# Optimization experiments

Measured on AMD Instinct MI355X. Metric: run time of the kernel, lower is better.

Reference implementation:

```python
import jax, jax.numpy as jnp
import numpy as np

N_NODES = 100000


def gcn_conv(x, edge_index, W, b):
    """PyG GCNConv: symmetric normalization with added self-loops.
    x: [N, Fin], edge_index: [2, E], W: [Fin, Fout], b: [Fout]
    """
    n = x.shape[0]
    h = x @ W  # [N, Fout] dense transform first (standard GCNConv order)
    loops = jnp.arange(n, dtype=edge_index.dtype)
    src = jnp.concatenate([edge_index[0], loops])  # self-loops appended
    dst = jnp.concatenate([edge_index[1], loops])
    deg = jax.ops.segment_sum(jnp.ones_like(dst, dtype=h.dtype), dst, num_segments=n)
    dinv = jax.lax.rsqrt(deg)  # deg >= 1 thanks to self-loops
    norm = dinv[src] * dinv[dst]  # [E+N]
    msgs = h[src] * norm[:, None]  # gather + scale
    out = jax.ops.segment_sum(msgs, dst, num_segments=n)  # scatter-add
    return out + b


def setup_inputs() -> dict:
    key = jax.random.key(0)
    k = jax.random.split(key, 9)
    in_c, hid, out_c = 128, 128, 64
    n_edges = 1600000
    x = jax.random.normal(k[0], (N_NODES, in_c), dtype=jnp.float32)
    edge_index = jax.random.randint(k[1], (2, n_edges), 0, N_NODES, dtype=jnp.int64)
    def lin(kw, kb, fan_in, fan_out):
        bound = 1.0 / np.sqrt(fan_in)
        W = jax.random.uniform(kw, (fan_in, fan_out), jnp.float32, -bound, bound)
        b = jax.random.uniform(kb, (fan_out,), jnp.float32, -bound, bound)
        return W, b
    W1, b1 = lin(k[2], k[3], in_c, hid)
    W2, b2 = lin(k[4], k[5], hid, hid)
    Wf, bf = lin(k[6], k[7], hid, out_c)
    return {"x": x, "edge_index": edge_index, "W1": W1, "b1": b1,
            "W2": W2, "b2": b2, "Wf": Wf, "bf": bf}


def reference(x, edge_index, W1, b1, W2, b2, Wf, bf):
    h = jax.nn.relu(gcn_conv(x, edge_index, W1, b1))
    h = jax.nn.relu(gcn_conv(h, edge_index, W2, b2))
    return h @ Wf + bf
```

## Files before the change

### kernel.cpp

```cpp
#include <hip/hip_runtime.h>
#include <stdint.h>

typedef short short8 __attribute__((ext_vector_type(8)));
typedef float floatx4 __attribute__((ext_vector_type(4)));

#define BK 256

static __device__ __forceinline__ float bflo(unsigned int u) {
    union { unsigned int i; float f; } v; v.i = u << 16; return v.f;
}
static __device__ __forceinline__ float bfhi(unsigned int u) {
    union { unsigned int i; float f; } v; v.i = u & 0xffff0000u; return v.f;
}
static __device__ __forceinline__ unsigned short f2bf(float f) {
    union { float f; unsigned int i; } v; v.f = f;
    unsigned int u = v.i;
    unsigned int r = u + 0x7fffu + ((u >> 16) & 1u);
    return (unsigned short)(r >> 16);
}


__global__ void k_zero_cnt(int* bucket_cnt, int K) {
    int i = blockIdx.x * 256 + threadIdx.x;
    if (i < K) bucket_cnt[i] = 0;
}

__global__ __launch_bounds__(256) void k_hist(const int* __restrict__ dst, int* bucket_cnt,
                                              int E, int N, int K) {
    __shared__ int h[4][512];
    int t = threadIdx.x, w = t >> 6;
    for (int i = t; i < 4 * 512; i += 256) ((int*)h)[i] = 0;
    __syncthreads();
    int per = (E + gridDim.x - 1) / gridDim.x;
    int lo = blockIdx.x * per, hi = min(lo + per, E);
    for (int e = lo + t; e < hi; e += 256) {
        unsigned int d = (unsigned int)dst[e];
        if (d < (unsigned int)N) atomicAdd(&h[w][d >> 8], 1);
    }
    __syncthreads();
    for (int i = t; i < K; i += 256) {
        int c = h[0][i] + h[1][i] + h[2][i] + h[3][i];
        if (c) atomicAdd(&bucket_cnt[i], c);
    }
}

__global__ void k_scanK(const int* __restrict__ bucket_cnt, int* bucket_off, int* bucket_cur,
                        int* row_start, int K, int N) {
    __shared__ int s[512];
    int t = threadIdx.x;
    int v = (t < K) ? bucket_cnt[t] : 0;
    s[t] = v; __syncthreads();
    for (int off = 1; off < 512; off <<= 1) {
        int x = (t >= off) ? s[t - off] : 0;
        __syncthreads();
        s[t] += x;
        __syncthreads();
    }
    if (t < K) { bucket_off[t] = s[t] - v; bucket_cur[t] = s[t] - v; }
    if (t == K - 1) { bucket_off[K] = s[t]; row_start[N] = s[t]; }
}

__global__ __launch_bounds__(256) void k_binscatter(const int* __restrict__ src,
                                                    const int* __restrict__ dst,
                                                    int* bucket_cur, unsigned int* __restrict__ tmp,
                                                    int E, int N, int K) {
    __shared__ int h[4][512];
    int t = threadIdx.x, w = t >> 6;
    for (int i = t; i < 4 * 512; i += 256) ((int*)h)[i] = 0;
    __syncthreads();
    int per = (E + gridDim.x - 1) / gridDim.x;
    int lo = blockIdx.x * per, hi = min(lo + per, E);
    for (int e = lo + t; e < hi; e += 256) {
        unsigned int d = (unsigned int)dst[e];
        if (d < (unsigned int)N) atomicAdd(&h[w][d >> 8], 1);
    }
    __syncthreads();
    for (int k = t; k < K; k += 256) {
        int c0 = h[0][k], c1 = h[1][k], c2 = h[2][k], c3 = h[3][k];
        int tot = c0 + c1 + c2 + c3;
        int base = tot ? atomicAdd(&bucket_cur[k], tot) : 0;
        h[0][k] = base; h[1][k] = base + c0; h[2][k] = base + c0 + c1;
        h[3][k] = base + c0 + c1 + c2;
    }
    __syncthreads();
    for (int e = lo + t; e < hi; e += 256) {
        unsigned int d = (unsigned int)dst[e];
        if (d < (unsigned int)N) {
            unsigned int sv = (unsigned int)src[e];
            if (sv >= (unsigned int)N) sv = 0;
            int p = atomicAdd(&h[w][d >> 8], 1);
            tmp[p] = (sv << 8) | (d & 255u);
        }
    }
}

__global__ __launch_bounds__(256) void k_fine(const unsigned int* __restrict__ tmp,
                                              const int* __restrict__ bucket_off,
                                              int* __restrict__ row_start, float* __restrict__ dinv,
                                              int* __restrict__ csr, int N) {
    __shared__ int deg4[4][BK];
    __shared__ int scn[BK];
    __shared__ int cur[BK];
    int b = blockIdx.x, t = threadIdx.x, w = t >> 6;
    int lo = bucket_off[b], hi = bucket_off[b + 1];
    for (int i = t; i < 4 * BK; i += 256) ((int*)deg4)[i] = 0;
    __syncthreads();
    for (int e = lo + t; e < hi; e += 256) atomicAdd(&deg4[w][tmp[e] & 255u], 1);
    __syncthreads();
    int v = deg4[0][t] + deg4[1][t] + deg4[2][t] + deg4[3][t];
    scn[t] = v; __syncthreads();
    for (int off = 1; off < 256; off <<= 1) {
        int x = (t >= off) ? scn[t - off] : 0;
        __syncthreads();
        scn[t] += x;
        __syncthreads();
    }
    int rs = lo + scn[t] - v;
    cur[t] = rs;
    int node = b * BK + t;
    if (node < N) { row_start[node] = rs; dinv[node] = rsqrtf((float)(v + 1)); }
    __syncthreads();
    for (int e = lo + t; e < hi; e += 256) {
        unsigned int p = tmp[e];
        int pos = atomicAdd(&cur[p & 255u], 1);
        csr[pos] = (int)(p >> 8);
    }
}


__global__ void k_wconv_all(const float* __restrict__ W1, const float* __restrict__ W2,
                            const float* __restrict__ Wf, unsigned short* __restrict__ wb1,
                            unsigned short* __restrict__ wb2, unsigned short* __restrict__ wbf) {
    int i = blockIdx.x * 256 + threadIdx.x;
    if (i < 16384) {
        int k = i >> 7, n = i & 127;
        wb1[n * 128 + k] = f2bf(W1[i]);
    } else if (i < 32768) {
        int j = i - 16384, k = j >> 7, n = j & 127;
        wb2[n * 128 + k] = f2bf(W2[j]);
    } else if (i < 40960) {
        int j = i - 32768, k = j >> 6, n = j & 63;
        wbf[n * 128 + k] = f2bf(Wf[j]);
    }
}


template <int NOUT, bool SCALE, bool BIAS, bool XF32, bool OUTF32>
__global__ __launch_bounds__(256, 2) void k_gemm(
    const void* __restrict__ Xv, const unsigned short* __restrict__ Wbf,
    const float* __restrict__ bias, const float* __restrict__ dinv,
    void* __restrict__ outv, int M, int MB) {
    __shared__ __align__(16) unsigned short Wl[NOUT * 136];
    int t = threadIdx.x;
    for (int c = t; c < NOUT * 16; c += 256) {
        short8 v = *(const short8*)(Wbf + (size_t)c * 8);
        *(short8*)(&Wl[(c >> 4) * 136 + (c & 15) * 8]) = v;
    }
    __syncthreads();

    int wave = t >> 6, lane = t & 63;
    int quad = lane >> 4, l16 = lane & 15;
    constexpr int NT = NOUT / 16;

    for (int mb = blockIdx.x; mb < MB; mb += gridDim.x) {
        int m0 = mb * 64 + wave * 16;
        int mr = m0 + l16;
        int mrc = mr < M ? mr : M - 1;

        floatx4 acc[NT];
#pragma unroll
        for (int i = 0; i < NT; i++) acc[i] = (floatx4){0.f, 0.f, 0.f, 0.f};

#pragma unroll
        for (int kc = 0; kc < 4; kc++) {
            short8 a;
            if (XF32) {
                const float* X = (const float*)Xv;
                const float* p = X + (size_t)mrc * 128 + kc * 32 + quad * 8;
                float4 xa = *(const float4*)p;
                float4 xb = *(const float4*)(p + 4);
                a[0] = (short)f2bf(xa.x); a[1] = (short)f2bf(xa.y);
                a[2] = (short)f2bf(xa.z); a[3] = (short)f2bf(xa.w);
                a[4] = (short)f2bf(xb.x); a[5] = (short)f2bf(xb.y);
                a[6] = (short)f2bf(xb.z); a[7] = (short)f2bf(xb.w);
            } else {
                const unsigned short* X = (const unsigned short*)Xv;
                a = *(const short8*)(X + (size_t)mrc * 128 + kc * 32 + quad * 8);
            }
#pragma unroll
            for (int nt = 0; nt < NT; nt++) {
                short8 b = *(const short8*)(&Wl[(nt * 16 + l16) * 136 + kc * 32 + quad * 8]);
                acc[nt] = __builtin_amdgcn_mfma_f32_16x16x32_bf16(a, b, acc[nt], 0, 0, 0);
            }
        }

#pragma unroll
        for (int i = 0; i < 4; i++) {
            int r = m0 + quad * 4 + i;
            if (r >= M) continue;
            float sc = SCALE ? dinv[r] : 1.0f;
#pragma unroll
            for (int nt = 0; nt < NT; nt++) {
                int n = nt * 16 + l16;
                float v = acc[nt][i] * sc;
                if (BIAS) v += bias[n];
                if (OUTF32) {
                    ((float*)outv)[(size_t)r * NOUT + n] = v;
                } else {
                    ((unsigned short*)outv)[(size_t)r * NOUT + n] = f2bf(v);
                }
            }
        }
    }
}


__global__ __launch_bounds__(256, 8) void k_aggregate(
    const unsigned short* __restrict__ Hs, const int* __restrict__ csr,
    const int* __restrict__ row_start,
    const float* __restrict__ dinv, const float* __restrict__ bias,
    unsigned short* __restrict__ out, int N, int E) {
    int wave = threadIdx.x >> 6, lane = threadIdx.x & 63;
    int grp = lane >> 4, c16 = lane & 15;
    int node = blockIdx.x * 4 + wave;
    if (node >= N) return;
    int Nm1 = N - 1;
    int cb = c16 * 8;

    float a0 = 0.f, a1 = 0.f, a2 = 0.f, a3 = 0.f, a4 = 0.f, a5 = 0.f, a6 = 0.f, a7 = 0.f;

    int start = row_start[node];
    int end = row_start[node + 1];
    if (start < 0) start = 0;
    if (end > E) end = E;
    int cnt = end - start;
    int full4 = cnt >> 2;

    int it = 0;
    for (; it + 2 <= full4; it += 2) {
        int eA = start + it * 4 + grp;
        int eB = eA + 4;
        int iA = min(max(csr[eA], 0), Nm1);
        int iB = min(max(csr[eB], 0), Nm1);
        uint4 uA = *(const uint4*)(Hs + (size_t)iA * 128 + cb);
        uint4 uB = *(const uint4*)(Hs + (size_t)iB * 128 + cb);
        a0 += bflo(uA.x); a1 += bfhi(uA.x); a2 += bflo(uA.y); a3 += bfhi(uA.y);
        a4 += bflo(uA.z); a5 += bfhi(uA.z); a6 += bflo(uA.w); a7 += bfhi(uA.w);
        a0 += bflo(uB.x); a1 += bfhi(uB.x); a2 += bflo(uB.y); a3 += bfhi(uB.y);
        a4 += bflo(uB.z); a5 += bfhi(uB.z); a6 += bflo(uB.w); a7 += bfhi(uB.w);
    }
    for (; it < full4; it++) {
        int eA = start + it * 4 + grp;
        int iA = min(max(csr[eA], 0), Nm1);
        uint4 uA = *(const uint4*)(Hs + (size_t)iA * 128 + cb);
        a0 += bflo(uA.x); a1 += bfhi(uA.x); a2 += bflo(uA.y); a3 += bfhi(uA.y);
        a4 += bflo(uA.z); a5 += bfhi(uA.z); a6 += bflo(uA.w); a7 += bfhi(uA.w);
    }
    int eT = start + full4 * 4 + grp;
    if (eT < end) {
        int iT = min(max(csr[eT], 0), Nm1);
        uint4 uT = *(const uint4*)(Hs + (size_t)iT * 128 + cb);
        a0 += bflo(uT.x); a1 += bfhi(uT.x); a2 += bflo(uT.y); a3 += bfhi(uT.y);
        a4 += bflo(uT.z); a5 += bfhi(uT.z); a6 += bflo(uT.w); a7 += bfhi(uT.w);
    }

    a0 += __shfl_xor(a0, 16); a1 += __shfl_xor(a1, 16); a2 += __shfl_xor(a2, 16);
    a3 += __shfl_xor(a3, 16); a4 += __shfl_xor(a4, 16); a5 += __shfl_xor(a5, 16);
    a6 += __shfl_xor(a6, 16); a7 += __shfl_xor(a7, 16);
    a0 += __shfl_xor(a0, 32); a1 += __shfl_xor(a1, 32); a2 += __shfl_xor(a2, 32);
    a3 += __shfl_xor(a3, 32); a4 += __shfl_xor(a4, 32); a5 += __shfl_xor(a5, 32);
    a6 += __shfl_xor(a6, 32); a7 += __shfl_xor(a7, 32);

    uint4 us = *(const uint4*)(Hs + (size_t)node * 128 + cb);
    a0 += bflo(us.x); a1 += bfhi(us.x); a2 += bflo(us.y); a3 += bfhi(us.y);
    a4 += bflo(us.z); a5 += bfhi(us.z); a6 += bflo(us.w); a7 += bfhi(us.w);

    float di = dinv[node];
    float4 b0 = *(const float4*)(bias + cb);
    float4 b1 = *(const float4*)(bias + cb + 4);
    float r0 = fmaxf(fmaf(di, a0, b0.x), 0.f);
    float r1 = fmaxf(fmaf(di, a1, b0.y), 0.f);
    float r2 = fmaxf(fmaf(di, a2, b0.z), 0.f);
    float r3 = fmaxf(fmaf(di, a3, b0.w), 0.f);
    float r4 = fmaxf(fmaf(di, a4, b1.x), 0.f);
    float r5 = fmaxf(fmaf(di, a5, b1.y), 0.f);
    float r6 = fmaxf(fmaf(di, a6, b1.z), 0.f);
    float r7 = fmaxf(fmaf(di, a7, b1.w), 0.f);
    if (grp == 0) {
        uint4 o;
        o.x = (unsigned int)f2bf(r0) | ((unsigned int)f2bf(r1) << 16);
        o.y = (unsigned int)f2bf(r2) | ((unsigned int)f2bf(r3) << 16);
        o.z = (unsigned int)f2bf(r4) | ((unsigned int)f2bf(r5) << 16);
        o.w = (unsigned int)f2bf(r6) | ((unsigned int)f2bf(r7) << 16);
        *(uint4*)(out + (size_t)node * 128 + cb) = o;
    }
}


extern "C" void kernel_launch(void* const* d_in, const int* in_sizes, int n_in,
                              void* d_out, int out_size, void* d_ws, size_t ws_size,
                              hipStream_t stream) {
    const float* x  = (const float*)d_in[0];
    const int* ei   = (const int*)d_in[1];
    const float* W1 = (const float*)d_in[2];
    const float* b1 = (const float*)d_in[3];
    const float* W2 = (const float*)d_in[4];
    const float* b2 = (const float*)d_in[5];
    const float* Wf = (const float*)d_in[6];
    const float* bf = (const float*)d_in[7];

    int N = in_sizes[0] / 128;
    int E = in_sizes[1] / 2;
    const int* src = ei;
    const int* dst = ei + E;
    int K = (N + BK - 1) / BK;
    if (N >= (1 << 24) || K > 512) return;

    size_t need = 0;
    auto pad = [](size_t b) { return (b + 255) & ~(size_t)255; };
    size_t o_bcnt = need; need += pad(512 * 4);
    size_t o_boff = need; need += pad(513 * 4);
    size_t o_bcur = need; need += pad(512 * 4);
    size_t o_rs   = need; need += pad(((size_t)N + 1) * 4);
    size_t o_dinv = need; need += pad((size_t)N * 4);
    size_t o_wbf  = need; need += pad((16384 + 16384 + 8192) * 2);
    size_t o_csr  = need; need += pad((size_t)E * 4);
    size_t o_hs   = need; need += pad((size_t)N * 128 * 2);
    size_t o_a    = need; need += pad((size_t)N * 128 * 2);
    if (ws_size < need) return;
    if ((size_t)E * 4 > (size_t)N * 128 * 2) return;

    char* ws = (char*)d_ws;
    int* bucket_cnt = (int*)(ws + o_bcnt);
    int* bucket_off = (int*)(ws + o_boff);
    int* bucket_cur = (int*)(ws + o_bcur);
    int* row_start  = (int*)(ws + o_rs);
    float* dinv     = (float*)(ws + o_dinv);
    unsigned short* wb1 = (unsigned short*)(ws + o_wbf);
    unsigned short* wb2 = wb1 + 16384;
    unsigned short* wbf = wb2 + 16384;
    int* csr        = (int*)(ws + o_csr);
    unsigned short* Hs = (unsigned short*)(ws + o_hs);
    unsigned short* A  = (unsigned short*)(ws + o_a);
    unsigned int* tmp  = (unsigned int*)A;

    k_wconv_all<<<160, 256, 0, stream>>>(W1, W2, Wf, wb1, wb2, wbf);

    k_zero_cnt<<<2, 256, 0, stream>>>(bucket_cnt, 512);
    k_hist<<<256, 256, 0, stream>>>(dst, bucket_cnt, E, N, K);
    k_scanK<<<1, 512, 0, stream>>>(bucket_cnt, bucket_off, bucket_cur, row_start, K, N);
    k_binscatter<<<256, 256, 0, stream>>>(src, dst, bucket_cur, tmp, E, N, K);
    k_fine<<<K, 256, 0, stream>>>(tmp, bucket_off, row_start, dinv, csr, N);

    int MB = (N + 63) / 64;
    int GG = (MB + 1) / 2;

    k_gemm<128, true, false, true, false><<<GG, 256, 0, stream>>>(x, wb1, nullptr, dinv, Hs, N, MB);
    k_aggregate<<<(N + 3) / 4, 256, 0, stream>>>(Hs, csr, row_start, dinv, b1, A, N, E);
    k_gemm<128, true, false, false, false><<<GG, 256, 0, stream>>>(A, wb2, nullptr, dinv, Hs, N, MB);
    k_aggregate<<<(N + 3) / 4, 256, 0, stream>>>(Hs, csr, row_start, dinv, b2, A, N, E);
    k_gemm<64, false, true, false, true><<<GG, 256, 0, stream>>>(A, wbf, bf, nullptr, d_out, N, MB);
}
```

Before: 336.5 us.

## Preload CSR indices per wave and broadcast via shuffles in aggregate kernel

The aggregate kernel now loads up to 64 neighbor indices once per wave, one per lane, and hands them to the gathering lanes with __shfl. This removes the dependent per-iteration CSR loads that preceded each feature-row gather. The main loop is unrolled to four gathers in flight, the self-row load is hoisted ahead of the loop, accumulation uses packed float2 vectors, and addresses are built with 32-bit shift/or arithmetic. Rows with more than 64 neighbors fall back to a direct CSR loop, and the 32-bit offsets assume the feature buffer stays under 4 GB.

```diff
diff --git a/kernel.cpp b/kernel.cpp
--- a/kernel.cpp
+++ b/kernel.cpp
@@ -3,6 +3,7 @@
 
 typedef short short8 __attribute__((ext_vector_type(8)));
 typedef float floatx4 __attribute__((ext_vector_type(4)));
+typedef float f32x2 __attribute__((ext_vector_type(2)));
 
 #define BK 256
 
@@ -17,6 +18,11 @@
     unsigned int u = v.i;
     unsigned int r = u + 0x7fffu + ((u >> 16) & 1u);
     return (unsigned short)(r >> 16);
+}
+static __device__ __forceinline__ f32x2 unp2(unsigned int u) {
+    union { unsigned int i; float f; } lo, hi;
+    lo.i = u << 16; hi.i = u & 0xffff0000u;
+    f32x2 r; r.x = lo.f; r.y = hi.f; return r;
 }
 
 
@@ -225,44 +231,59 @@
     int node = blockIdx.x * 4 + wave;
     if (node >= N) return;
     int Nm1 = N - 1;
-    int cb = c16 * 8;
-
-    float a0 = 0.f, a1 = 0.f, a2 = 0.f, a3 = 0.f, a4 = 0.f, a5 = 0.f, a6 = 0.f, a7 = 0.f;
+    unsigned int cb2 = (unsigned int)c16 << 4;
+    const char* Hb = (const char*)Hs;
 
     int start = row_start[node];
     int end = row_start[node + 1];
     if (start < 0) start = 0;
     if (end > E) end = E;
     int cnt = end - start;
-    int full4 = cnt >> 2;
-
+
+    uint4 us = *(const uint4*)(Hb + (((size_t)node << 8) | cb2));
+
+    int pre = cnt < 64 ? cnt : 64;
+    int idxv = 0;
+    if (lane < pre) idxv = min(max(csr[start + lane], 0), Nm1);
+
+    f32x2 a01 = {0.f, 0.f}, a23 = {0.f, 0.f}, a45 = {0.f, 0.f}, a67 = {0.f, 0.f};
+#define ACC8(u) do { a01 += unp2((u).x); a23 += unp2((u).y); \
+                     a45 += unp2((u).z); a67 += unp2((u).w); } while (0)
+
+    int full4 = pre >> 2;
     int it = 0;
-    for (; it + 2 <= full4; it += 2) {
-        int eA = start + it * 4 + grp;
-        int eB = eA + 4;
-        int iA = min(max(csr[eA], 0), Nm1);
-        int iB = min(max(csr[eB], 0), Nm1);
-        uint4 uA = *(const uint4*)(Hs + (size_t)iA * 128 + cb);
-        uint4 uB = *(const uint4*)(Hs + (size_t)iB * 128 + cb);
-        a0 += bflo(uA.x); a1 += bfhi(uA.x); a2 += bflo(uA.y); a3 += bfhi(uA.y);
-        a4 += bflo(uA.z); a5 += bfhi(uA.z); a6 += bflo(uA.w); a7 += bfhi(uA.w);
-        a0 += bflo(uB.x); a1 += bfhi(uB.x); a2 += bflo(uB.y); a3 += bfhi(uB.y);
-        a4 += bflo(uB.z); a5 += bfhi(uB.z); a6 += bflo(uB.w); a7 += bfhi(uB.w);
+    for (; it + 4 <= full4; it += 4) {
+        int p = it * 4 + grp;
+        int i0 = __shfl(idxv, p);
+        int i1 = __shfl(idxv, p + 4);
+        int i2 = __shfl(idxv, p + 8);
+        int i3 = __shfl(idxv, p + 12);
+        uint4 u0 = *(const uint4*)(Hb + (((unsigned int)i0 << 8) | cb2));
+        uint4 u1 = *(const uint4*)(Hb + (((unsigned int)i1 << 8) | cb2));
+        uint4 u2 = *(const uint4*)(Hb + (((unsigned int)i2 << 8) | cb2));
+        uint4 u3 = *(const uint4*)(Hb + (((unsigned int)i3 << 8) | cb2));
+        ACC8(u0); ACC8(u1); ACC8(u2); ACC8(u3);
     }
     for (; it < full4; it++) {
-        int eA = start + it * 4 + grp;
-        int iA = min(max(csr[eA], 0), Nm1);
-        uint4 uA = *(const uint4*)(Hs + (size_t)iA * 128 + cb);
-        a0 += bflo(uA.x); a1 += bfhi(uA.x); a2 += bflo(uA.y); a3 += bfhi(uA.y);
-        a4 += bflo(uA.z); a5 += bfhi(uA.z); a6 += bflo(uA.w); a7 += bfhi(uA.w);
-    }
-    int eT = start + full4 * 4 + grp;
-    if (eT < end) {
-        int iT = min(max(csr[eT], 0), Nm1);
-        uint4 uT = *(const uint4*)(Hs + (size_t)iT * 128 + cb);
-        a0 += bflo(uT.x); a1 += bfhi(uT.x); a2 += bflo(uT.y); a3 += bfhi(uT.y);
-        a4 += bflo(uT.z); a5 += bfhi(uT.z); a6 += bflo(uT.w); a7 += bfhi(uT.w);
-    }
+        int i0 = __shfl(idxv, it * 4 + grp);
+        uint4 u0 = *(const uint4*)(Hb + (((unsigned int)i0 << 8) | cb2));
+        ACC8(u0);
+    }
+    int eT = full4 * 4 + grp;
+    int iT = __shfl(idxv, eT < pre ? eT : 0);
+    if (eT < pre) {
+        uint4 u0 = *(const uint4*)(Hb + (((unsigned int)iT << 8) | cb2));
+        ACC8(u0);
+    }
+    for (int e = start + 64 + grp; e < end; e += 4) {
+        int ii = min(max(csr[e], 0), Nm1);
+        uint4 u = *(const uint4*)(Hb + (((unsigned int)ii << 8) | cb2));
+        ACC8(u);
+    }
+#undef ACC8
+
+    float a0 = a01.x, a1 = a01.y, a2 = a23.x, a3 = a23.y;
+    float a4 = a45.x, a5 = a45.y, a6 = a67.x, a7 = a67.y;
 
     a0 += __shfl_xor(a0, 16); a1 += __shfl_xor(a1, 16); a2 += __shfl_xor(a2, 16);
     a3 += __shfl_xor(a3, 16); a4 += __shfl_xor(a4, 16); a5 += __shfl_xor(a5, 16);
@@ -271,13 +292,12 @@
     a3 += __shfl_xor(a3, 32); a4 += __shfl_xor(a4, 32); a5 += __shfl_xor(a5, 32);
     a6 += __shfl_xor(a6, 32); a7 += __shfl_xor(a7, 32);
 
-    uint4 us = *(const uint4*)(Hs + (size_t)node * 128 + cb);
     a0 += bflo(us.x); a1 += bfhi(us.x); a2 += bflo(us.y); a3 += bfhi(us.y);
     a4 += bflo(us.z); a5 += bfhi(us.z); a6 += bflo(us.w); a7 += bfhi(us.w);
 
     float di = dinv[node];
-    float4 b0 = *(const float4*)(bias + cb);
-    float4 b1 = *(const float4*)(bias + cb + 4);
+    float4 b0 = *(const float4*)(bias + c16 * 8);
+    float4 b1 = *(const float4*)(bias + c16 * 8 + 4);
     float r0 = fmaxf(fmaf(di, a0, b0.x), 0.f);
     float r1 = fmaxf(fmaf(di, a1, b0.y), 0.f);
     float r2 = fmaxf(fmaf(di, a2, b0.z), 0.f);
@@ -292,7 +312,7 @@
         o.y = (unsigned int)f2bf(r2) | ((unsigned int)f2bf(r3) << 16);
         o.z = (unsigned int)f2bf(r4) | ((unsigned int)f2bf(r5) << 16);
         o.w = (unsigned int)f2bf(r6) | ((unsigned int)f2bf(r7) << 16);
-        *(uint4*)(out + (size_t)node * 128 + cb) = o;
+        *(uint4*)(out + (((size_t)node << 7) | (size_t)(c16 * 8))) = o;
     }
 }
 
```

Result: no change. 335.9 us (-0.2%).

## Store features in 16-column slices and aggregate per slice for cache locality

Applied to the files above, without the earlier changes.

Changes the intermediate feature layout to eight column slices of 16 bf16 values per node. The GEMMs write and read this sliced layout, and the new aggregation kernel launches one block per (node chunk, slice) so each gather touches a 3.2MB slice that fits in cache better. Each lane takes a different edge and the results are combined with a 16-lane shuffle reduction. The change also folds the bucket-count zeroing into the weight-conversion kernel to save a launch. In exchange, the CSR indices are re-read once per slice (8x index traffic), the GEMM stores become strided, and there is more shuffle work.

```diff
diff --git a/kernel.cpp b/kernel.cpp
--- a/kernel.cpp
+++ b/kernel.cpp
@@ -20,9 +20,22 @@
 }
 
 
-__global__ void k_zero_cnt(int* bucket_cnt, int K) {
+__global__ void k_wconv_all(const float* __restrict__ W1, const float* __restrict__ W2,
+                            const float* __restrict__ Wf, unsigned short* __restrict__ wb1,
+                            unsigned short* __restrict__ wb2, unsigned short* __restrict__ wbf,
+                            int* __restrict__ bucket_cnt) {
     int i = blockIdx.x * 256 + threadIdx.x;
-    if (i < K) bucket_cnt[i] = 0;
+    if (i < 512) bucket_cnt[i] = 0;
+    if (i < 16384) {
+        int k = i >> 7, n = i & 127;
+        wb1[n * 128 + k] = f2bf(W1[i]);
+    } else if (i < 32768) {
+        int j = i - 16384, k = j >> 7, n = j & 127;
+        wb2[n * 128 + k] = f2bf(W2[j]);
+    } else if (i < 40960) {
+        int j = i - 32768, k = j >> 6, n = j & 63;
+        wbf[n * 128 + k] = f2bf(Wf[j]);
+    }
 }
 
 __global__ __launch_bounds__(256) void k_hist(const int* __restrict__ dst, int* bucket_cnt,
@@ -128,24 +141,7 @@
 }
 
 
-__global__ void k_wconv_all(const float* __restrict__ W1, const float* __restrict__ W2,
-                            const float* __restrict__ Wf, unsigned short* __restrict__ wb1,
-                            unsigned short* __restrict__ wb2, unsigned short* __restrict__ wbf) {
-    int i = blockIdx.x * 256 + threadIdx.x;
-    if (i < 16384) {
-        int k = i >> 7, n = i & 127;
-        wb1[n * 128 + k] = f2bf(W1[i]);
-    } else if (i < 32768) {
-        int j = i - 16384, k = j >> 7, n = j & 127;
-        wb2[n * 128 + k] = f2bf(W2[j]);
-    } else if (i < 40960) {
-        int j = i - 32768, k = j >> 6, n = j & 63;
-        wbf[n * 128 + k] = f2bf(Wf[j]);
-    }
-}
-
-
-template <int NOUT, bool SCALE, bool BIAS, bool XF32, bool OUTF32>
+template <int NOUT, bool SCALE, bool BIAS, bool XF32, bool XSLICED, bool OUTF32, bool OSLICED>
 __global__ __launch_bounds__(256, 2) void k_gemm(
     const void* __restrict__ Xv, const unsigned short* __restrict__ Wbf,
     const float* __restrict__ bias, const float* __restrict__ dinv,
@@ -183,6 +179,10 @@
                 a[2] = (short)f2bf(xa.z); a[3] = (short)f2bf(xa.w);
                 a[4] = (short)f2bf(xb.x); a[5] = (short)f2bf(xb.y);
                 a[6] = (short)f2bf(xb.z); a[7] = (short)f2bf(xb.w);
+            } else if (XSLICED) {
+                const unsigned short* X = (const unsigned short*)Xv;
+                int sl = kc * 2 + (quad >> 1);
+                a = *(const short8*)(X + ((size_t)sl * M + mrc) * 16 + (quad & 1) * 8);
             } else {
                 const unsigned short* X = (const unsigned short*)Xv;
                 a = *(const short8*)(X + (size_t)mrc * 128 + kc * 32 + quad * 8);
@@ -206,6 +206,8 @@
                 if (BIAS) v += bias[n];
                 if (OUTF32) {
                     ((float*)outv)[(size_t)r * NOUT + n] = v;
+                } else if (OSLICED) {
+                    ((unsigned short*)outv)[((size_t)nt * M + r) * 16 + l16] = f2bf(v);
                 } else {
                     ((unsigned short*)outv)[(size_t)r * NOUT + n] = f2bf(v);
                 }
@@ -215,84 +217,93 @@
 }
 
 
-__global__ __launch_bounds__(256, 8) void k_aggregate(
+__global__ __launch_bounds__(256, 8) void k_agg_slice(
     const unsigned short* __restrict__ Hs, const int* __restrict__ csr,
-    const int* __restrict__ row_start,
-    const float* __restrict__ dinv, const float* __restrict__ bias,
-    unsigned short* __restrict__ out, int N, int E) {
-    int wave = threadIdx.x >> 6, lane = threadIdx.x & 63;
-    int grp = lane >> 4, c16 = lane & 15;
-    int node = blockIdx.x * 4 + wave;
-    if (node >= N) return;
+    const int* __restrict__ row_start, const float* __restrict__ dinv,
+    const float* __restrict__ bias, unsigned short* __restrict__ out, int N, int E) {
+    int s = blockIdx.x & 7, chunk = blockIdx.x >> 3;
+    int t = threadIdx.x;
+    int wave = t >> 6, lane = t & 63, sub = lane >> 4, el = lane & 15;
     int Nm1 = N - 1;
-    int cb = c16 * 8;
-
-    float a0 = 0.f, a1 = 0.f, a2 = 0.f, a3 = 0.f, a4 = 0.f, a5 = 0.f, a6 = 0.f, a7 = 0.f;
-
-    int start = row_start[node];
-    int end = row_start[node + 1];
-    if (start < 0) start = 0;
-    if (end > E) end = E;
-    int cnt = end - start;
-    int full4 = cnt >> 2;
-
-    int it = 0;
-    for (; it + 2 <= full4; it += 2) {
-        int eA = start + it * 4 + grp;
-        int eB = eA + 4;
-        int iA = min(max(csr[eA], 0), Nm1);
-        int iB = min(max(csr[eB], 0), Nm1);
-        uint4 uA = *(const uint4*)(Hs + (size_t)iA * 128 + cb);
-        uint4 uB = *(const uint4*)(Hs + (size_t)iB * 128 + cb);
-        a0 += bflo(uA.x); a1 += bfhi(uA.x); a2 += bflo(uA.y); a3 += bfhi(uA.y);
-        a4 += bflo(uA.z); a5 += bfhi(uA.z); a6 += bflo(uA.w); a7 += bfhi(uA.w);
-        a0 += bflo(uB.x); a1 += bfhi(uB.x); a2 += bflo(uB.y); a3 += bfhi(uB.y);
-        a4 += bflo(uB.z); a5 += bfhi(uB.z); a6 += bflo(uB.w); a7 += bfhi(uB.w);
-    }
-    for (; it < full4; it++) {
-        int eA = start + it * 4 + grp;
-        int iA = min(max(csr[eA], 0), Nm1);
-        uint4 uA = *(const uint4*)(Hs + (size_t)iA * 128 + cb);
-        a0 += bflo(uA.x); a1 += bfhi(uA.x); a2 += bflo(uA.y); a3 += bfhi(uA.y);
-        a4 += bflo(uA.z); a5 += bfhi(uA.z); a6 += bflo(uA.w); a7 += bfhi(uA.w);
-    }
-    int eT = start + full4 * 4 + grp;
-    if (eT < end) {
-        int iT = min(max(csr[eT], 0), Nm1);
-        uint4 uT = *(const uint4*)(Hs + (size_t)iT * 128 + cb);
-        a0 += bflo(uT.x); a1 += bfhi(uT.x); a2 += bflo(uT.y); a3 += bfhi(uT.y);
-        a4 += bflo(uT.z); a5 += bfhi(uT.z); a6 += bflo(uT.w); a7 += bfhi(uT.w);
-    }
-
-    a0 += __shfl_xor(a0, 16); a1 += __shfl_xor(a1, 16); a2 += __shfl_xor(a2, 16);
-    a3 += __shfl_xor(a3, 16); a4 += __shfl_xor(a4, 16); a5 += __shfl_xor(a5, 16);
-    a6 += __shfl_xor(a6, 16); a7 += __shfl_xor(a7, 16);
-    a0 += __shfl_xor(a0, 32); a1 += __shfl_xor(a1, 32); a2 += __shfl_xor(a2, 32);
-    a3 += __shfl_xor(a3, 32); a4 += __shfl_xor(a4, 32); a5 += __shfl_xor(a5, 32);
-    a6 += __shfl_xor(a6, 32); a7 += __shfl_xor(a7, 32);
-
-    uint4 us = *(const uint4*)(Hs + (size_t)node * 128 + cb);
-    a0 += bflo(us.x); a1 += bfhi(us.x); a2 += bflo(us.y); a3 += bfhi(us.y);
-    a4 += bflo(us.z); a5 += bfhi(us.z); a6 += bflo(us.w); a7 += bfhi(us.w);
-
-    float di = dinv[node];
-    float4 b0 = *(const float4*)(bias + cb);
-    float4 b1 = *(const float4*)(bias + cb + 4);
-    float r0 = fmaxf(fmaf(di, a0, b0.x), 0.f);
-    float r1 = fmaxf(fmaf(di, a1, b0.y), 0.f);
-    float r2 = fmaxf(fmaf(di, a2, b0.z), 0.f);
-    float r3 = fmaxf(fmaf(di, a3, b0.w), 0.f);
-    float r4 = fmaxf(fmaf(di, a4, b1.x), 0.f);
-    float r5 = fmaxf(fmaf(di, a5, b1.y), 0.f);
-    float r6 = fmaxf(fmaf(di, a6, b1.z), 0.f);
-    float r7 = fmaxf(fmaf(di, a7, b1.w), 0.f);
-    if (grp == 0) {
-        uint4 o;
-        o.x = (unsigned int)f2bf(r0) | ((unsigned int)f2bf(r1) << 16);
-        o.y = (unsigned int)f2bf(r2) | ((unsigned int)f2bf(r3) << 16);
-        o.z = (unsigned int)f2bf(r4) | ((unsigned int)f2bf(r5) << 16);
-        o.w = (unsigned int)f2bf(r6) | ((unsigned int)f2bf(r7) << 16);
-        *(uint4*)(out + (size_t)node * 128 + cb) = o;
+    const unsigned short* Hsl = Hs + (size_t)s * N * 16;
+    unsigned short* Osl = out + (size_t)s * N * 16;
+
+    const float* bsl = bias + s * 16;
+    float4 q0 = *(const float4*)(bsl);
+    float4 q1 = *(const float4*)(bsl + 4);
+    float4 q2 = *(const float4*)(bsl + 8);
+    float4 q3 = *(const float4*)(bsl + 12);
+
+    int nb = chunk * 64 + wave * 16 + sub;
+#pragma unroll 1
+    for (int p = 0; p < 4; ++p) {
+        int node = nb + p * 4;
+        int node_c = node < N ? node : Nm1;
+        int start = row_start[node_c];
+        int end = row_start[node_c + 1];
+        if (start < 0) start = 0;
+        if (end > E) end = E;
+
+        float a0 = 0.f, a1 = 0.f, a2 = 0.f, a3 = 0.f, a4 = 0.f, a5 = 0.f, a6 = 0.f, a7 = 0.f;
+        float a8 = 0.f, a9 = 0.f, a10 = 0.f, a11 = 0.f, a12 = 0.f, a13 = 0.f, a14 = 0.f, a15 = 0.f;
+
+        for (int e = start + el; e < end; e += 16) {
+            unsigned int ii = (unsigned int)csr[e];
+            if (ii >= (unsigned int)N) ii = 0;
+            const uint4* rp = (const uint4*)(Hsl + (size_t)ii * 16);
+            uint4 ua = rp[0], ub = rp[1];
+            a0 += bflo(ua.x); a1 += bfhi(ua.x); a2 += bflo(ua.y); a3 += bfhi(ua.y);
+            a4 += bflo(ua.z); a5 += bfhi(ua.z); a6 += bflo(ua.w); a7 += bfhi(ua.w);
+            a8 += bflo(ub.x); a9 += bfhi(ub.x); a10 += bflo(ub.y); a11 += bfhi(ub.y);
+            a12 += bflo(ub.z); a13 += bfhi(ub.z); a14 += bflo(ub.w); a15 += bfhi(ub.w);
+        }
+
+#define RED(W) \
+        a0 += __shfl_xor(a0, W); a1 += __shfl_xor(a1, W); a2 += __shfl_xor(a2, W); \
+        a3 += __shfl_xor(a3, W); a4 += __shfl_xor(a4, W); a5 += __shfl_xor(a5, W); \
+        a6 += __shfl_xor(a6, W); a7 += __shfl_xor(a7, W); a8 += __shfl_xor(a8, W); \
+        a9 += __shfl_xor(a9, W); a10 += __shfl_xor(a10, W); a11 += __shfl_xor(a11, W); \
+        a12 += __shfl_xor(a12, W); a13 += __shfl_xor(a13, W); a14 += __shfl_xor(a14, W); \
+        a15 += __shfl_xor(a15, W);
+        RED(1) RED(2) RED(4) RED(8)
+#undef RED
+
+        if (el == 0 && node < N) {
+            const uint4* sp = (const uint4*)(Hsl + (size_t)node * 16);
+            uint4 sa = sp[0], sb = sp[1];
+            a0 += bflo(sa.x); a1 += bfhi(sa.x); a2 += bflo(sa.y); a3 += bfhi(sa.y);
+            a4 += bflo(sa.z); a5 += bfhi(sa.z); a6 += bflo(sa.w); a7 += bfhi(sa.w);
+            a8 += bflo(sb.x); a9 += bfhi(sb.x); a10 += bflo(sb.y); a11 += bfhi(sb.y);
+            a12 += bflo(sb.z); a13 += bfhi(sb.z); a14 += bflo(sb.w); a15 += bfhi(sb.w);
+            float di = dinv[node];
+            float r0 = fmaxf(fmaf(di, a0, q0.x), 0.f);
+            float r1 = fmaxf(fmaf(di, a1, q0.y), 0.f);
+            float r2 = fmaxf(fmaf(di, a2, q0.z), 0.f);
+            float r3 = fmaxf(fmaf(di, a3, q0.w), 0.f);
+            float r4 = fmaxf(fmaf(di, a4, q1.x), 0.f);
+            float r5 = fmaxf(fmaf(di, a5, q1.y), 0.f);
+            float r6 = fmaxf(fmaf(di, a6, q1.z), 0.f);
+            float r7 = fmaxf(fmaf(di, a7, q1.w), 0.f);
+            float r8 = fmaxf(fmaf(di, a8, q2.x), 0.f);
+            float r9 = fmaxf(fmaf(di, a9, q2.y), 0.f);
+            float r10 = fmaxf(fmaf(di, a10, q2.z), 0.f);
+            float r11 = fmaxf(fmaf(di, a11, q2.w), 0.f);
+            float r12 = fmaxf(fmaf(di, a12, q3.x), 0.f);
+            float r13 = fmaxf(fmaf(di, a13, q3.y), 0.f);
+            float r14 = fmaxf(fmaf(di, a14, q3.z), 0.f);
+            float r15 = fmaxf(fmaf(di, a15, q3.w), 0.f);
+            uint4 o0, o1;
+            o0.x = (unsigned int)f2bf(r0) | ((unsigned int)f2bf(r1) << 16);
+            o0.y = (unsigned int)f2bf(r2) | ((unsigned int)f2bf(r3) << 16);
+            o0.z = (unsigned int)f2bf(r4) | ((unsigned int)f2bf(r5) << 16);
+            o0.w = (unsigned int)f2bf(r6) | ((unsigned int)f2bf(r7) << 16);
+            o1.x = (unsigned int)f2bf(r8) | ((unsigned int)f2bf(r9) << 16);
+            o1.y = (unsigned int)f2bf(r10) | ((unsigned int)f2bf(r11) << 16);
+            o1.z = (unsigned int)f2bf(r12) | ((unsigned int)f2bf(r13) << 16);
+            o1.w = (unsigned int)f2bf(r14) | ((unsigned int)f2bf(r15) << 16);
+            *(uint4*)(Osl + (size_t)node * 16) = o0;
+            *(uint4*)(Osl + (size_t)node * 16 + 8) = o1;
+        }
     }
 }
 
@@ -344,9 +355,7 @@
     unsigned short* A  = (unsigned short*)(ws + o_a);
     unsigned int* tmp  = (unsigned int*)A;
 
-    k_wconv_all<<<160, 256, 0, stream>>>(W1, W2, Wf, wb1, wb2, wbf);
-
-    k_zero_cnt<<<2, 256, 0, stream>>>(bucket_cnt, 512);
+    k_wconv_all<<<160, 256, 0, stream>>>(W1, W2, Wf, wb1, wb2, wbf, bucket_cnt);
     k_hist<<<256, 256, 0, stream>>>(dst, bucket_cnt, E, N, K);
     k_scanK<<<1, 512, 0, stream>>>(bucket_cnt, bucket_off, bucket_cur, row_start, K, N);
     k_binscatter<<<256, 256, 0, stream>>>(src, dst, bucket_cur, tmp, E, N, K);
@@ -354,10 +363,14 @@
 
     int MB = (N + 63) / 64;
     int GG = (MB + 1) / 2;
-
-    k_gemm<128, true, false, true, false><<<GG, 256, 0, stream>>>(x, wb1, nullptr, dinv, Hs, N, MB);
-    k_aggregate<<<(N + 3) / 4, 256, 0, stream>>>(Hs, csr, row_start, dinv, b1, A, N, E);
-    k_gemm<128, true, false, false, false><<<GG, 256, 0, stream>>>(A, wb2, nullptr, dinv, Hs, N, MB);
-    k_aggregate<<<(N + 3) / 4, 256, 0, stream>>>(Hs, csr, row_start, dinv, b2, A, N, E);
-    k_gemm<64, false, true, false, true><<<GG, 256, 0, stream>>>(A, wbf, bf, nullptr, d_out, N, MB);
-}
+    int AGG = ((N + 63) / 64) * 8;
+
+    k_gemm<128, true, false, true, false, false, true><<<GG, 256, 0, stream>>>(
+        x, wb1, nullptr, dinv, Hs, N, MB);
+    k_agg_slice<<<AGG, 256, 0, stream>>>(Hs, csr, row_start, dinv, b1, A, N, E);
+    k_gemm<128, true, false, false, true, false, true><<<GG, 256, 0, stream>>>(
+        A, wb2, nullptr, dinv, Hs, N, MB);
+    k_agg_slice<<<AGG, 256, 0, stream>>>(Hs, csr, row_start, dinv, b2, A, N, E);
+    k_gemm<64, false, true, false, true, true, false><<<GG, 256, 0, stream>>>(
+        A, wbf, bf, nullptr, d_out, N, MB);
+}
```

Result: slower. 485.5 us (+44.3%).
